# Kernel tuning notes

Hardware: AMD Instinct MI355X
Metric: run time of the kernel (lower is better)

The kernel has to match this reference:

```python
import jax, jax.numpy as jnp
import numpy as np

D = 1024          # model_dim
BD = D // 2       # bottleneck_dim
K = 64            # num_splats
B, S = 8, 2048


def setup_inputs() -> dict:
    key = jax.random.key(0)
    ks = jax.random.split(key, 12)
    sc = 0.02
    return {
        "token_embeddings": jax.random.normal(ks[0], (B, S, D), jnp.float32),
        "splat_influences": jax.random.uniform(ks[1], (B, S, K), jnp.float32),
        # encoder: Linear(D -> BD), stored [in, out]
        "enc_W": jax.random.normal(ks[2], (D, BD), jnp.float32) * sc,
        "enc_b": jnp.zeros((BD,), jnp.float32),
        # per-splat transforms: K x Linear(BD -> BD)
        "trans_W": jax.random.normal(ks[3], (K, BD, BD), jnp.float32) * sc,
        "trans_b": jnp.zeros((K, BD), jnp.float32),
        # decoder: Linear(BD -> D)
        "dec_W": jax.random.normal(ks[4], (BD, D), jnp.float32) * sc,
        "dec_b": jnp.zeros((D,), jnp.float32),
        # flow gate: Linear(D -> D) + sigmoid
        "gate_W": jax.random.normal(ks[5], (D, D), jnp.float32) * sc,
        "gate_b": jnp.zeros((D,), jnp.float32),
    }


def reference(token_embeddings, splat_influences, enc_W, enc_b,
              trans_W, trans_b, dec_W, dec_b, gate_W, gate_b):
    # gather: [B,K,S] @ [B,S,D] -> [B,K,D]
    influences_t = jnp.swapaxes(splat_influences, 1, 2)          # [B,K,S]
    gathered = jnp.einsum('bks,bsd->bkd', influences_t, token_embeddings)
    total = jnp.clip(influences_t.sum(axis=2, keepdims=True), 1e-8, None)  # [B,K,1]
    gathered = gathered / total
    # encoder (dropout inactive at eval)
    encoded = jax.nn.relu(gathered @ enc_W + enc_b)              # [B,K,BD]
    # per-splat transform as grouped matmul
    transformed = jnp.einsum('bkd,kde->bke', encoded, trans_W) + trans_b  # [B,K,BD]
    decoded = transformed @ dec_W + dec_b                        # [B,K,D]
    # scatter back to tokens: [B,S,K] @ [B,K,D]
    flow = jnp.einsum('bsk,bkd->bsd', splat_influences, decoded)
    gate = jax.nn.sigmoid(token_embeddings @ gate_W + gate_b)    # [B,S,D]
    return flow * gate
```

## Files before the change

kernel.cpp:

```cpp
#include <hip/hip_runtime.h>

#define BB 8
#define SS 2048
#define DD 1024
#define BDD 512
#define NSP 64

typedef __attribute__((ext_vector_type(8))) short bf16x8;
typedef __attribute__((ext_vector_type(4))) float f32x4;
typedef unsigned short u16;
typedef unsigned int u32;

__device__ __forceinline__ u16 f2bf(float f) {
  u32 u = __builtin_bit_cast(u32, f);
  u = u + 0x7fffu + ((u >> 16) & 1u);
  return (u16)(u >> 16);
}

__device__ __forceinline__ void gl_lds16(const void* g, void* l) {
  __builtin_amdgcn_global_load_lds((const __attribute__((address_space(1))) void*)g,
                                   (__attribute__((address_space(3))) void*)l,
                                   16, 0, 0);
}

__global__ void k_prep(const float* __restrict__ tok, const float* __restrict__ infl,
                       const float* __restrict__ gw, u16* __restrict__ tokbf,
                       u16* __restrict__ tokT, u16* __restrict__ inflbf,
                       u16* __restrict__ inflT, float* __restrict__ rsum,
                       u16* __restrict__ gwt) {
  __shared__ __align__(16) char smraw[128 * 41 * 4];
  u16(*tile)[80] = (u16(*)[80])smraw;
  float(*ps)[64] = (float(*)[64])(smraw + 64 * 80 * 2);
  float(*gt)[33] = (float(*)[33])smraw;
  int bid = blockIdx.x;
  int t = threadIdx.x;

  if (bid < 2048) {
    u32* t32 = (u32*)smraw;
    int C0 = (bid & 15) * 64;
    int R0 = (bid >> 4) * 128;
    int b = R0 >> 11, s0 = R0 & 2047;
    int lc = (t & 7) * 8;
#pragma unroll
    for (int i = 0; i < 4; ++i) {
      int r = (t >> 3) + i * 32;
      const float* src = tok + (size_t)(R0 + r) * DD + C0 + lc;
      float4 a = *(const float4*)src;
      float4 bq = *(const float4*)(src + 4);
      uint4 v;
      v.x = f2bf(a.x) | ((u32)f2bf(a.y) << 16);
      v.y = f2bf(a.z) | ((u32)f2bf(a.w) << 16);
      v.z = f2bf(bq.x) | ((u32)f2bf(bq.y) << 16);
      v.w = f2bf(bq.z) | ((u32)f2bf(bq.w) << 16);
      *(uint4*)(tokbf + (size_t)(R0 + r) * DD + C0 + lc) = v;
      int cbase = r * 41 + (t & 7) * 4;
      t32[cbase + 0] = v.x;
      t32[cbase + 1] = v.y;
      t32[cbase + 2] = v.z;
      t32[cbase + 3] = v.w;
    }
    __syncthreads();
    int dp = t >> 3;
    size_t tb = (size_t)b * DD * SS;
#pragma unroll
    for (int h = 0; h < 2; ++h) {
      int sseg = (t & 7) * 8 + h * 64;
      u32 w[8];
#pragma unroll
      for (int j = 0; j < 8; ++j) w[j] = t32[(sseg + j) * 41 + dp];
      uint4 vlo, vhi;
      vlo.x = (w[0] & 0xffffu) | (w[1] << 16);
      vlo.y = (w[2] & 0xffffu) | (w[3] << 16);
      vlo.z = (w[4] & 0xffffu) | (w[5] << 16);
      vlo.w = (w[6] & 0xffffu) | (w[7] << 16);
      vhi.x = (w[0] >> 16) | (w[1] & 0xffff0000u);
      vhi.y = (w[2] >> 16) | (w[3] & 0xffff0000u);
      vhi.z = (w[4] >> 16) | (w[5] & 0xffff0000u);
      vhi.w = (w[6] >> 16) | (w[7] & 0xffff0000u);
      *(uint4*)(tokT + tb + (size_t)(C0 + 2 * dp) * SS + s0 + sseg) = vlo;
      *(uint4*)(tokT + tb + (size_t)(C0 + 2 * dp + 1) * SS + s0 + sseg) = vhi;
    }
  } else if (bid < 2304) {
    int R0 = (bid - 2048) * 64;
    int b = R0 >> 11, s0 = R0 & 2047;
    int st = s0 >> 6;
    int lr = t >> 3, lc = (t & 7) * 8;
    float col[8];
#pragma unroll
    for (int j = 0; j < 8; ++j) col[j] = 0.f;
#pragma unroll
    for (int i = 0; i < 2; ++i) {
      int r = lr + i * 32;
      const float* src = infl + (size_t)(R0 + r) * NSP + lc;
      float4 a = *(const float4*)src;
      float4 bq = *(const float4*)(src + 4);
      col[0] += a.x; col[1] += a.y; col[2] += a.z; col[3] += a.w;
      col[4] += bq.x; col[5] += bq.y; col[6] += bq.z; col[7] += bq.w;
      uint4 v;
      v.x = f2bf(a.x) | ((u32)f2bf(a.y) << 16);
      v.y = f2bf(a.z) | ((u32)f2bf(a.w) << 16);
      v.z = f2bf(bq.x) | ((u32)f2bf(bq.y) << 16);
      v.w = f2bf(bq.z) | ((u32)f2bf(bq.w) << 16);
      *(uint4*)(inflbf + (size_t)(R0 + r) * NSP + lc) = v;
      *(uint4*)&tile[r][lc] = v;
    }
#pragma unroll
    for (int j = 0; j < 8; ++j) ps[lr][lc + j] = col[j];
    __syncthreads();
    if (t < 64) {
      float s = 0.f;
#pragma unroll
      for (int rr = 0; rr < 32; ++rr) s += ps[rr][t];
      rsum[((size_t)b * 32 + st) * 64 + t] = s;
    }
    int sseg = (t & 7) * 8;
#pragma unroll
    for (int i = 0; i < 2; ++i) {
      int dcol = (t >> 3) + i * 32;
      u16 a0 = tile[sseg + 0][dcol], a1 = tile[sseg + 1][dcol];
      u16 a2 = tile[sseg + 2][dcol], a3 = tile[sseg + 3][dcol];
      u16 a4 = tile[sseg + 4][dcol], a5 = tile[sseg + 5][dcol];
      u16 a6 = tile[sseg + 6][dcol], a7 = tile[sseg + 7][dcol];
      uint4 v;
      v.x = a0 | ((u32)a1 << 16);
      v.y = a2 | ((u32)a3 << 16);
      v.z = a4 | ((u32)a5 << 16);
      v.w = a6 | ((u32)a7 << 16);
      *(uint4*)(inflT + ((size_t)b * NSP + dcol) * SS + s0 + sseg) = v;
    }
  } else {
    int g = bid - 2304;
    int n0 = (g & 31) * 32, k0 = (g >> 5) * 32;
    int tx = t & 31, ty = t >> 5;
#pragma unroll
    for (int r = 0; r < 4; ++r) {
      int kr = ty + r * 8;
      gt[kr][tx] = gw[(k0 + kr) * DD + n0 + tx];
    }
    __syncthreads();
#pragma unroll
    for (int r = 0; r < 4; ++r) {
      int nc = ty + r * 8;
      gwt[(n0 + nc) * DD + k0 + tx] = f2bf(gt[tx][nc]);
    }
  }
}

__global__ __launch_bounds__(256) void k_gather_mfma(const u16* __restrict__ inflT,
                                                     const u16* __restrict__ tokT,
                                                     float* __restrict__ pg) {
  __shared__ u16 As[64 * 64];
  __shared__ u16 Bs[64 * 64];
  int t = threadIdx.x;
  int l = t & 63, w = t >> 6;
  int wr = w >> 1, wc = w & 1;
  int n0 = blockIdx.x * 64;
  int b = blockIdx.y;
  int sq = blockIdx.z;
  int l15 = l & 15, lh = l >> 4;
  int srow = t >> 3, scol = (t & 7) * 8;

  const u16* ap = inflT + (size_t)b * NSP * SS;
  const u16* bp = tokT + (size_t)b * DD * SS;

  f32x4 acc[2][2];
#pragma unroll
  for (int i = 0; i < 2; ++i)
#pragma unroll
    for (int j = 0; j < 2; ++j) acc[i][j] = (f32x4){0.f, 0.f, 0.f, 0.f};

  for (int kt = 0; kt < 8; ++kt) {
    int k0 = sq * 512 + kt * 64;
#pragma unroll
    for (int i = 0; i < 2; ++i) {
      int row = srow + i * 32;
      gl_lds16(ap + row * SS + k0 + scol, &As[row * 64 + scol]);
      gl_lds16(bp + (n0 + row) * SS + k0 + scol, &Bs[row * 64 + scol]);
    }
    __syncthreads();
#pragma unroll
    for (int ks = 0; ks < 2; ++ks) {
      bf16x8 af[2], bfv[2];
#pragma unroll
      for (int mi = 0; mi < 2; ++mi)
        af[mi] = *(const bf16x8*)&As[(wr * 32 + mi * 16 + l15) * 64 + ks * 32 + lh * 8];
#pragma unroll
      for (int ni = 0; ni < 2; ++ni)
        bfv[ni] = *(const bf16x8*)&Bs[(wc * 32 + ni * 16 + l15) * 64 + ks * 32 + lh * 8];
#pragma unroll
      for (int mi = 0; mi < 2; ++mi)
#pragma unroll
        for (int ni = 0; ni < 2; ++ni)
          acc[mi][ni] = __builtin_amdgcn_mfma_f32_16x16x32_bf16(af[mi], bfv[ni], acc[mi][ni], 0, 0, 0);
    }
    __syncthreads();
  }

#pragma unroll
  for (int mi = 0; mi < 2; ++mi)
#pragma unroll
    for (int ni = 0; ni < 2; ++ni)
#pragma unroll
      for (int r = 0; r < 4; ++r) {
        int krow = wr * 32 + mi * 16 + lh * 4 + r;
        int dcol = n0 + wc * 32 + ni * 16 + l15;
        pg[((size_t)sq * 512 + b * NSP + krow) * DD + dcol] = acc[mi][ni][r];
      }
}

__global__ void k_enc_part(const float* __restrict__ pg, const float* __restrict__ rsum,
                           const float* __restrict__ encW, float* __restrict__ pe) {
  __shared__ float gl[8][64];
  int dq = blockIdx.x, mt = blockIdx.y;
  int m0 = mt * 8, d0 = dq * 64;
  int t = threadIdx.x;
  {
    int r = t >> 5, c = t & 31;
    float s1 = 0.f, s2 = 0.f;
#pragma unroll
    for (int q = 0; q < 4; ++q) {
      const float* qp = pg + ((size_t)q * 512 + m0 + r) * DD + d0;
      s1 += qp[c]; s2 += qp[c + 32];
    }
    int mrow = m0 + r;
    int bq = mrow >> 6, kq = mrow & 63;
    float tt = 0.f;
#pragma unroll
    for (int st = 0; st < 32; ++st) tt += rsum[((size_t)bq * 32 + st) * 64 + kq];
    float rt = 1.f / fmaxf(tt, 1e-8f);
    gl[r][c] = s1 * rt;
    gl[r][c + 32] = s2 * rt;
  }
  __syncthreads();
  int n4 = (t & 127) * 4, mh = (t >> 7) * 4;
  float4 acc[4];
#pragma unroll
  for (int m = 0; m < 4; ++m) acc[m] = (float4){0.f, 0.f, 0.f, 0.f};
  for (int i = 0; i < 64; ++i) {
    float4 wv = *(const float4*)(encW + (d0 + i) * BDD + n4);
#pragma unroll
    for (int m = 0; m < 4; ++m) {
      float g = gl[mh + m][i];
      acc[m].x += g * wv.x; acc[m].y += g * wv.y;
      acc[m].z += g * wv.z; acc[m].w += g * wv.w;
    }
  }
#pragma unroll
  for (int m = 0; m < 4; ++m)
    *(float4*)(pe + ((size_t)dq * 512 + m0 + mh + m) * BDD + n4) = acc[m];
}

__global__ void k_trans_part(const float* __restrict__ pe, const float* __restrict__ encB,
                             const float* __restrict__ trW, float* __restrict__ pt) {
  __shared__ float el[8][32];
  int dq = blockIdx.x, ks = blockIdx.y;
  int d0 = dq * 32;
  int t = threadIdx.x;
  {
    int r = t >> 5, c = t & 31;
    int m = r * NSP + ks;
    float s = 0.f;
#pragma unroll
    for (int p = 0; p < 16; ++p)
      s += pe[((size_t)p * 512 + m) * BDD + d0 + c];
    el[r][c] = fmaxf(s + encB[d0 + c], 0.f);
  }
  __syncthreads();
  int n4 = (t & 127) * 4, mh = (t >> 7) * 4;
  float4 acc[4];
#pragma unroll
  for (int m = 0; m < 4; ++m) acc[m] = (float4){0.f, 0.f, 0.f, 0.f};
  for (int i = 0; i < 32; ++i) {
    float4 wv = *(const float4*)(trW + ((size_t)ks * BDD + d0 + i) * BDD + n4);
#pragma unroll
    for (int m = 0; m < 4; ++m) {
      float g = el[mh + m][i];
      acc[m].x += g * wv.x; acc[m].y += g * wv.y;
      acc[m].z += g * wv.z; acc[m].w += g * wv.w;
    }
  }
#pragma unroll
  for (int m = 0; m < 4; ++m)
    *(float4*)(pt + ((size_t)dq * 512 + (mh + m) * NSP + ks) * BDD + n4) = acc[m];
}

__global__ void k_dec_part(const float* __restrict__ pt, const float* __restrict__ trB,
                           const float* __restrict__ decW, float* __restrict__ pd) {
  __shared__ float tl[8][64];
  int dq = blockIdx.x, mt = blockIdx.y;
  int m0 = mt * 8, d0 = dq * 64;
  int t = threadIdx.x;
  {
    int r = t >> 5, c = t & 31;
    int m = m0 + r;
    float s1 = 0.f, s2 = 0.f;
#pragma unroll
    for (int p = 0; p < 16; ++p) {
      const float* qp = pt + ((size_t)p * 512 + m) * BDD + d0;
      s1 += qp[c]; s2 += qp[c + 32];
    }
    tl[r][c] = s1 + trB[(m & 63) * BDD + d0 + c];
    tl[r][c + 32] = s2 + trB[(m & 63) * BDD + d0 + c + 32];
  }
  __syncthreads();
  int n4 = t * 4;
  float4 acc[8];
#pragma unroll
  for (int m = 0; m < 8; ++m) acc[m] = (float4){0.f, 0.f, 0.f, 0.f};
  for (int i = 0; i < 64; ++i) {
    float4 wv = *(const float4*)(decW + (d0 + i) * DD + n4);
#pragma unroll
    for (int m = 0; m < 8; ++m) {
      float g = tl[m][i];
      acc[m].x += g * wv.x; acc[m].y += g * wv.y;
      acc[m].z += g * wv.z; acc[m].w += g * wv.w;
    }
  }
#pragma unroll
  for (int m = 0; m < 8; ++m)
    *(float4*)(pd + ((size_t)dq * 512 + m0 + m) * DD + n4) = acc[m];
}

__global__ void red_dec(const float* __restrict__ pd, const float* __restrict__ decB,
                        u16* __restrict__ decT) {
  __shared__ u16 st[64][34];
  int nt = blockIdx.x, b = blockIdx.y;
  int n0 = nt * 32;
  int t = threadIdx.x;
  int nn = t & 31, kg = t >> 5;
  float db = decB[n0 + nn];
#pragma unroll
  for (int ki = 0; ki < 8; ++ki) {
    int ks = kg * 8 + ki;
    float s = db;
#pragma unroll
    for (int p = 0; p < 8; ++p)
      s += pd[((size_t)p * 512 + b * NSP + ks) * DD + n0 + nn];
    st[ks][nn] = f2bf(s);
  }
  __syncthreads();
  int nr = t >> 3, kseg = (t & 7) * 8;
  uint4 v;
  v.x = st[kseg + 0][nr] | ((u32)st[kseg + 1][nr] << 16);
  v.y = st[kseg + 2][nr] | ((u32)st[kseg + 3][nr] << 16);
  v.z = st[kseg + 4][nr] | ((u32)st[kseg + 5][nr] << 16);
  v.w = st[kseg + 6][nr] | ((u32)st[kseg + 7][nr] << 16);
  *(uint4*)(decT + ((size_t)b * DD + n0 + nr) * NSP + kseg) = v;
}


#define GVM(n) asm volatile("s_waitcnt vmcnt(" #n ")" ::: "memory");

#define GSTA(sl, k0, p)                                                        \
  { int e = (p)*512 + t; int row = e >> 3; int cs = ((e & 7) ^ (row & 7)) * 8; \
    gl_lds16(tokbf + (size_t)(m0 + row) * DD + (k0) + cs, &As[sl][e * 8]); }
#define GSTB(sl, k0, p)                                                        \
  { int e = (p)*512 + t; int row = e >> 3; int cs = ((e & 7) ^ (row & 7)) * 8; \
    gl_lds16(gwt + (size_t)(n0 + row) * DD + (k0) + cs, &Bs[sl][e * 8]); }
#define SAI(sl, p)                                                             \
  { int e = (p)*512 + t; int row = e >> 3; int cs = ((e & 7) ^ (row & 7)) * 8; \
    gl_lds16(inflbf + ((size_t)bb * SS + s0m + row) * NSP + cs, &As[sl][e * 8]); }
#define SBD(sl, p)                                                             \
  { int e = (p)*512 + t; int row = e >> 3; int cs = ((e & 7) ^ (row & 7)) * 8; \
    gl_lds16(decT + ((size_t)bb * DD + n0 + row) * NSP + cs, &Bs[sl][e * 8]); }

#define GLOADB(sl)                                                             \
  _Pragma("unroll")                                                            \
  for (int nf = 0; nf < 2; ++nf) {                                             \
    int br = wc * 32 + nf * 16 + l15;                                          \
    bfv[nf][0] = *(const bf16x8*)&Bs[sl][br * 64 + c0];                        \
    bfv[nf][1] = *(const bf16x8*)&Bs[sl][br * 64 + c1];                        \
  }

#define GPH(sl, mq, VMW, STG, LDB)                                             \
  {                                                                            \
    VMW                                                                        \
    __builtin_amdgcn_s_barrier();                                              \
    LDB                                                                        \
    bf16x8 af[4][2];                                                           \
    _Pragma("unroll")                                                          \
    for (int mf = 0; mf < 4; ++mf) {                                           \
      int ar = (mq)*64 + mf * 16 + l15;                                        \
      af[mf][0] = *(const bf16x8*)&As[sl][ar * 64 + c0];                       \
      af[mf][1] = *(const bf16x8*)&As[sl][ar * 64 + c1];                       \
    }                                                                          \
    STG                                                                        \
    __builtin_amdgcn_s_setprio(1);                                             \
    _Pragma("unroll")                                                          \
    for (int mf = 0; mf < 4; ++mf)                                             \
      _Pragma("unroll")                                                        \
      for (int nf = 0; nf < 2; ++nf) {                                         \
        acc[(mq)*4 + mf][nf] = __builtin_amdgcn_mfma_f32_16x16x32_bf16(af[mf][0], bfv[nf][0], acc[(mq)*4 + mf][nf], 0, 0, 0); \
        acc[(mq)*4 + mf][nf] = __builtin_amdgcn_mfma_f32_16x16x32_bf16(af[mf][1], bfv[nf][1], acc[(mq)*4 + mf][nf], 0, 0, 0); \
      }                                                                        \
    __builtin_amdgcn_s_setprio(0);                                             \
    __builtin_amdgcn_s_barrier();                                              \
  }

#define GT_FULL(sl, osl, k1)                                                   \
  {                                                                            \
    bf16x8 bfv[2][2];                                                          \
    GPH(sl, 0, GVM(3), GSTB(osl, k1, 0) GSTB(osl, k1, 1), GLOADB(sl))          \
    GPH(sl, 1, GVM(4), GSTB(osl, k1, 2) GSTB(osl, k1, 3), )                    \
    GPH(sl, 2, GVM(5), GSTA(osl, k1, 0) GSTA(osl, k1, 1), )                    \
    GPH(sl, 3, GVM(6), GSTA(osl, k1, 2) GSTA(osl, k1, 3), )                    \
  }
#define GT_LAST(sl)                                                            \
  {                                                                            \
    bf16x8 bfv[2][2];                                                          \
    GPH(sl, 0, GVM(3), , GLOADB(sl))                                           \
    GPH(sl, 1, GVM(2), , )                                                     \
    GPH(sl, 2, GVM(1), , )                                                     \
    GPH(sl, 3, GVM(0), , )                                                     \
  }
#define GT_SCAT(sl)                                                            \
  {                                                                            \
    bf16x8 bfv[2][2];                                                          \
    GPH(sl, 0, , , GLOADB(sl))                                                 \
    GPH(sl, 1, , , )                                                           \
    GPH(sl, 2, , , )                                                           \
    GPH(sl, 3, , , )                                                           \
  }

__global__ __launch_bounds__(512, 1) void k_gate(const u16* __restrict__ tokbf,
                                                 const u16* __restrict__ gwt,
                                                 const u16* __restrict__ inflbf,
                                                 const u16* __restrict__ decT,
                                                 const float* __restrict__ gateB,
                                                 float* __restrict__ outp) {
  __shared__ u16 As[2][256 * 64];
  __shared__ u16 Bs[2][256 * 64];
  int t = threadIdx.x;
  int l = t & 63, wc = t >> 6;
  int bid = blockIdx.x;
  int wg = (bid & 7) * 32 + (bid >> 3);
  int mt = wg & 63, nt = wg >> 6;
  int m0 = mt * 256, n0 = nt * 256;
  int l15 = l & 15, lh = l >> 4;
  int x7 = l15 & 7;
  int c0 = (lh ^ x7) * 8;
  int c1 = ((4 + lh) ^ x7) * 8;
  int bb = m0 >> 11, s0m = m0 & 2047;

  f32x4 acc[16][2];
#pragma unroll
  for (int i = 0; i < 16; ++i)
#pragma unroll
    for (int j = 0; j < 2; ++j) acc[i][j] = (f32x4){0.f, 0.f, 0.f, 0.f};

  GSTB(0, 0, 0) GSTB(0, 0, 1) GSTB(0, 0, 2) GSTB(0, 0, 3)
  GSTA(0, 0, 0) GSTA(0, 0, 1) GSTA(0, 0, 2) GSTA(0, 0, 3)

#pragma unroll 1
  for (int i = 0; i < 7; ++i) {
    GT_FULL(0, 1, (2 * i + 1) * 64)
    GT_FULL(1, 0, (2 * i + 2) * 64)
  }
  GT_FULL(0, 1, 960)
  GT_LAST(1)

  SAI(0, 0) SAI(0, 1) SAI(0, 2) SAI(0, 3)
  SBD(0, 0) SBD(0, 1) SBD(0, 2) SBD(0, 3)

  u32 zp[16][2][2];
#pragma unroll
  for (int a = 0; a < 16; ++a)
#pragma unroll
    for (int nf = 0; nf < 2; ++nf) {
      zp[a][nf][0] = f2bf(acc[a][nf][0]) | ((u32)f2bf(acc[a][nf][1]) << 16);
      zp[a][nf][1] = f2bf(acc[a][nf][2]) | ((u32)f2bf(acc[a][nf][3]) << 16);
    }
#pragma unroll
  for (int i = 0; i < 16; ++i)
#pragma unroll
    for (int j = 0; j < 2; ++j) acc[i][j] = (f32x4){0.f, 0.f, 0.f, 0.f};
  GVM(0)
  __builtin_amdgcn_s_barrier();

  GT_SCAT(0)

  float gb[2];
#pragma unroll
  for (int nf = 0; nf < 2; ++nf) gb[nf] = gateB[n0 + wc * 32 + nf * 16 + l15];
#pragma unroll
  for (int a = 0; a < 16; ++a)
#pragma unroll
    for (int nf = 0; nf < 2; ++nf)
#pragma unroll
      for (int r = 0; r < 4; ++r) {
        int mr = m0 + a * 16 + lh * 4 + r;
        int nc = n0 + wc * 32 + nf * 16 + l15;
        u32 wz = zp[a][nf][r >> 1];
        u32 h = (r & 1) ? (wz & 0xffff0000u) : (wz << 16);
        float z = __builtin_bit_cast(float, h) + gb[nf];
        float gate = 1.f / (1.f + __expf(-z));
        outp[(size_t)mr * DD + nc] = acc[a][nf][r] * gate;
      }
}

extern "C" void kernel_launch(void* const* d_in, const int* in_sizes, int n_in,
                              void* d_out, int out_size, void* d_ws, size_t ws_size,
                              hipStream_t stream) {
  const float* tok = (const float*)d_in[0];
  const float* infl = (const float*)d_in[1];
  const float* encW = (const float*)d_in[2];
  const float* encB = (const float*)d_in[3];
  const float* trW = (const float*)d_in[4];
  const float* trB = (const float*)d_in[5];
  const float* decW = (const float*)d_in[6];
  const float* decB = (const float*)d_in[7];
  const float* gw = (const float*)d_in[8];
  const float* gateB = (const float*)d_in[9];
  float* outp = (float*)d_out;

  char* wsp = (char*)d_ws;
  u16* tokbf = (u16*)(wsp);
  u16* gwt = (u16*)(wsp + 33554432);
  u16* inflbf = (u16*)(wsp + 35651584);
  u16* decT = (u16*)(wsp + 41945088);
  u16* tokT = (u16*)(wsp + 42993664);
  float* pe = (float*)(wsp + 42993664);
  float* pt = (float*)(wsp + 42993664 + 16777216);
  u16* inflT = (u16*)(wsp + 76548096);
  float* rsum = (float*)(wsp + 78645248);
  float* scratch = (float*)(wsp + 78710784);

  k_prep<<<dim3(3328), dim3(256), 0, stream>>>(tok, infl, gw, tokbf, tokT, inflbf,
                                               inflT, rsum, gwt);
  k_gather_mfma<<<dim3(16, 8, 4), dim3(256), 0, stream>>>(inflT, tokT, scratch);
  k_enc_part<<<dim3(16, 64), dim3(256), 0, stream>>>(scratch, rsum, encW, pe);
  k_trans_part<<<dim3(16, 64), dim3(256), 0, stream>>>(pe, encB, trW, pt);
  k_dec_part<<<dim3(8, 64), dim3(256), 0, stream>>>(pt, trB, decW, scratch);
  red_dec<<<dim3(32, 8), dim3(256), 0, stream>>>(scratch, decB, decT);
  k_gate<<<dim3(256), dim3(512), 0, stream>>>(tokbf, gwt, inflbf, decT, gateB, outp);
}
```

Measured before the change: 170.3 us.

## Overlap scatter-operand staging with last gate K-step and fuse scatter epilogue

The staging of scatter operands (influences and decoded matrix) into shared memory is moved into the final gate-GEMM K iteration so it overlaps with MFMA work instead of running afterwards. The scatter GEMM is now computed per 64-row quarter with a small separate accumulator and written out immediately. This keeps the gate logits in fp32 registers rather than packing them to bf16. The goal is to shorten the serialized tail of the kernel, at the cost of higher register pressure from holding the full gate accumulator plus extra scatter accumulators.

Measured after the change: 158.0 us. 1.08x faster.

```diff
diff --git a/kernel.cpp b/kernel.cpp
--- a/kernel.cpp
+++ b/kernel.cpp
@@ -405,21 +405,13 @@
     GPH(sl, 2, GVM(5), GSTA(osl, k1, 0) GSTA(osl, k1, 1), )                    \
     GPH(sl, 3, GVM(6), GSTA(osl, k1, 2) GSTA(osl, k1, 3), )                    \
   }
-#define GT_LAST(sl)                                                            \
+#define GT_LAST2(sl)                                                           \
   {                                                                            \
     bf16x8 bfv[2][2];                                                          \
-    GPH(sl, 0, GVM(3), , GLOADB(sl))                                           \
-    GPH(sl, 1, GVM(2), , )                                                     \
-    GPH(sl, 2, GVM(1), , )                                                     \
-    GPH(sl, 3, GVM(0), , )                                                     \
-  }
-#define GT_SCAT(sl)                                                            \
-  {                                                                            \
-    bf16x8 bfv[2][2];                                                          \
-    GPH(sl, 0, , , GLOADB(sl))                                                 \
-    GPH(sl, 1, , , )                                                           \
-    GPH(sl, 2, , , )                                                           \
-    GPH(sl, 3, , , )                                                           \
+    GPH(sl, 0, GVM(3), SAI(0, 0) SAI(0, 1), GLOADB(sl))                        \
+    GPH(sl, 1, GVM(4), SAI(0, 2) SAI(0, 3), )                                  \
+    GPH(sl, 2, GVM(5), SBD(0, 0) SBD(0, 1), )                                  \
+    GPH(sl, 3, GVM(6), SBD(0, 2) SBD(0, 3), )                                  \
   }
 
 __global__ __launch_bounds__(512, 1) void k_gate(const u16* __restrict__ tokbf,
@@ -457,45 +449,54 @@
     GT_FULL(1, 0, (2 * i + 2) * 64)
   }
   GT_FULL(0, 1, 960)
-  GT_LAST(1)
-
-  SAI(0, 0) SAI(0, 1) SAI(0, 2) SAI(0, 3)
-  SBD(0, 0) SBD(0, 1) SBD(0, 2) SBD(0, 3)
-
-  u32 zp[16][2][2];
-#pragma unroll
-  for (int a = 0; a < 16; ++a)
-#pragma unroll
-    for (int nf = 0; nf < 2; ++nf) {
-      zp[a][nf][0] = f2bf(acc[a][nf][0]) | ((u32)f2bf(acc[a][nf][1]) << 16);
-      zp[a][nf][1] = f2bf(acc[a][nf][2]) | ((u32)f2bf(acc[a][nf][3]) << 16);
-    }
-#pragma unroll
-  for (int i = 0; i < 16; ++i)
-#pragma unroll
-    for (int j = 0; j < 2; ++j) acc[i][j] = (f32x4){0.f, 0.f, 0.f, 0.f};
+  GT_LAST2(1)
+
   GVM(0)
   __builtin_amdgcn_s_barrier();
 
-  GT_SCAT(0)
-
-  float gb[2];
-#pragma unroll
-  for (int nf = 0; nf < 2; ++nf) gb[nf] = gateB[n0 + wc * 32 + nf * 16 + l15];
-#pragma unroll
-  for (int a = 0; a < 16; ++a)
-#pragma unroll
-    for (int nf = 0; nf < 2; ++nf)
-#pragma unroll
-      for (int r = 0; r < 4; ++r) {
-        int mr = m0 + a * 16 + lh * 4 + r;
-        int nc = n0 + wc * 32 + nf * 16 + l15;
-        u32 wz = zp[a][nf][r >> 1];
-        u32 h = (r & 1) ? (wz & 0xffff0000u) : (wz << 16);
-        float z = __builtin_bit_cast(float, h) + gb[nf];
-        float gate = 1.f / (1.f + __expf(-z));
-        outp[(size_t)mr * DD + nc] = acc[a][nf][r] * gate;
+  {
+    float gb[2];
+#pragma unroll
+    for (int nf = 0; nf < 2; ++nf) gb[nf] = gateB[n0 + wc * 32 + nf * 16 + l15];
+    bf16x8 bfv[2][2];
+    GLOADB(0)
+#pragma unroll
+    for (int mq = 0; mq < 4; ++mq) {
+      bf16x8 af[4][2];
+#pragma unroll
+      for (int mf = 0; mf < 4; ++mf) {
+        int ar = mq * 64 + mf * 16 + l15;
+        af[mf][0] = *(const bf16x8*)&As[0][ar * 64 + c0];
+        af[mf][1] = *(const bf16x8*)&As[0][ar * 64 + c1];
       }
+      f32x4 accf[4][2];
+#pragma unroll
+      for (int mf = 0; mf < 4; ++mf)
+#pragma unroll
+        for (int nf = 0; nf < 2; ++nf) accf[mf][nf] = (f32x4){0.f, 0.f, 0.f, 0.f};
+      __builtin_amdgcn_s_setprio(1);
+#pragma unroll
+      for (int mf = 0; mf < 4; ++mf)
+#pragma unroll
+        for (int nf = 0; nf < 2; ++nf) {
+          accf[mf][nf] = __builtin_amdgcn_mfma_f32_16x16x32_bf16(af[mf][0], bfv[nf][0], accf[mf][nf], 0, 0, 0);
+          accf[mf][nf] = __builtin_amdgcn_mfma_f32_16x16x32_bf16(af[mf][1], bfv[nf][1], accf[mf][nf], 0, 0, 0);
+        }
+      __builtin_amdgcn_s_setprio(0);
+#pragma unroll
+      for (int mf = 0; mf < 4; ++mf)
+#pragma unroll
+        for (int nf = 0; nf < 2; ++nf)
+#pragma unroll
+          for (int r = 0; r < 4; ++r) {
+            int mr = m0 + (mq * 4 + mf) * 16 + lh * 4 + r;
+            int nc = n0 + wc * 32 + nf * 16 + l15;
+            float z = acc[mq * 4 + mf][nf][r] + gb[nf];
+            float gate = 1.f / (1.f + __expf(-z));
+            outp[(size_t)mr * DD + nc] = accf[mf][nf][r] * gate;
+          }
+    }
+  }
 }
 
 extern "C" void kernel_launch(void* const* d_in, const int* in_sizes, int n_in,
```
